# Kernel tuning notes

Hardware: AMD Instinct MI355X
Metric: run time of the kernel (lower is better)

Reference implementation:

```python
import jax, jax.numpy as jnp
import numpy as np

DIM = 1024
HEADS = 16
WIN = 16
N = WIN * WIN + 1  # 257, CLS + patches
NUM_REL = (2 * WIN - 1) * (2 * WIN - 1) + 3  # 964
B = 64


def _build_rel_pos_index(w):
    coords = np.stack(np.meshgrid(np.arange(w), np.arange(w), indexing='ij'))  # [2,w,w]
    cf = coords.reshape(2, -1)  # [2, w*w]
    rel = cf[:, :, None] - cf[:, None, :]  # [2, ww, ww]
    rel = rel.transpose(1, 2, 0).astype(np.int64)
    rel[..., 0] += w - 1
    rel[..., 1] += w - 1
    rel[..., 0] *= 2 * w - 1
    nrd = (2 * w - 1) * (2 * w - 1) + 3
    idx = np.zeros((w * w + 1, w * w + 1), dtype=np.int32)
    idx[1:, 1:] = rel.sum(-1)
    idx[0, :] = nrd - 3
    idx[:, 0] = nrd - 2
    idx[0, 0] = nrd - 1
    return idx


def setup_inputs() -> dict:
    key = jax.random.key(0)
    ks = jax.random.split(key, 4)
    x = jax.random.normal(ks[0], (B, N, DIM), dtype=jnp.float32)
    qkv_w = jax.random.normal(ks[1], (3 * DIM, DIM), dtype=jnp.float32) * 0.02
    q_bias = jnp.zeros((DIM,), dtype=jnp.float32)
    v_bias = jnp.zeros((DIM,), dtype=jnp.float32)
    rel_pos_table = jax.random.normal(ks[2], (NUM_REL, HEADS), dtype=jnp.float32) * 0.02
    proj_w = jax.random.normal(ks[3], (DIM, DIM), dtype=jnp.float32) * 0.02
    proj_b = jnp.zeros((DIM,), dtype=jnp.float32)
    rel_pos_index = jnp.asarray(_build_rel_pos_index(WIN))
    attn_mask = jnp.ones((B, N), dtype=jnp.bool_)
    return {"x": x, "qkv_w": qkv_w, "q_bias": q_bias, "v_bias": v_bias,
            "rel_pos_table": rel_pos_table, "proj_w": proj_w, "proj_b": proj_b,
            "rel_pos_index": rel_pos_index, "attn_mask": attn_mask}


def reference(x, qkv_w, q_bias, v_bias, rel_pos_table, proj_w, proj_b, rel_pos_index, attn_mask):
    b, n, c = x.shape
    head_dim = c // HEADS
    scale = head_dim ** -0.5
    # qkv with q_bias / zero k bias / v_bias
    qkv_bias = jnp.concatenate([q_bias, jnp.zeros_like(v_bias), v_bias])
    qkv = x @ qkv_w.T + qkv_bias  # [B,N,3C]
    qkv = qkv.reshape(b, n, 3, HEADS, head_dim).transpose(2, 0, 3, 1, 4)  # [3,B,H,N,d]
    q, k, v = qkv[0], qkv[1], qkv[2]
    # fp32 upcast for scores (qk_float=True)
    attn = jnp.einsum('bhqd,bhkd->bhqk', (q * scale).astype(jnp.float32), k.astype(jnp.float32))
    # gathered relative position bias: table[idx] -> [N,N,H] -> [H,N,N]
    rel_bias = rel_pos_table[rel_pos_index].transpose(2, 0, 1)  # [H,N,N]
    attn = attn + rel_bias[None].astype(attn.dtype)
    attn = jnp.where(attn_mask[:, None, None, :], attn, -jnp.inf)
    attn = jax.nn.softmax(attn, axis=-1).astype(x.dtype)
    out = jnp.einsum('bhqk,bhkd->bhqd', attn, v)  # [B,H,N,d]
    out = out.transpose(0, 2, 1, 3).reshape(b, n, -1)  # [B,N,C]
    return out @ proj_w.T + proj_b
```

## Files before the change

kernel.cpp:

```cpp
#include <hip/hip_runtime.h>


typedef __attribute__((ext_vector_type(8))) short bf16x8;
typedef __attribute__((ext_vector_type(4))) float f32x4;

#define MFMA16(A, B, C) __builtin_amdgcn_mfma_f32_16x16x32_bf16((A), (B), (C), 0, 0, 0)

#define MV   16448
#define KDIM 1024
#define SEQ  257
#define SEQP 272
#define VCOLS 320

__device__ __forceinline__ void gll16(void* lds, const void* g) {
    __builtin_amdgcn_global_load_lds(
        (const __attribute__((address_space(1))) void*)g,
        (__attribute__((address_space(3))) void*)lds,
        16, 0, 0);
}

__device__ __forceinline__ unsigned short f2bf(float f) {
    union { float f; unsigned int u; } x;
    x.f = f;
    unsigned int r = x.u + 0x7FFFu + ((x.u >> 16) & 1u);
    return (unsigned short)(r >> 16);
}

__global__ __launch_bounds__(256) void prep_k(
    const float* __restrict__ x, const float* __restrict__ wq, const float* __restrict__ wp,
    const float* __restrict__ table, const int* __restrict__ rpi,
    unsigned short* __restrict__ xb, unsigned short* __restrict__ wqb,
    unsigned short* __restrict__ wpb, float* __restrict__ biasb)
{
    const int XT = MV * KDIM / 4;
    const int QT = 3072 * KDIM / 4;
    const int PT = KDIM * KDIM / 4;
    const int total = XT + QT + PT;
    for (int i = blockIdx.x * blockDim.x + threadIdx.x; i < total; i += gridDim.x * blockDim.x) {
        const float4* s; unsigned short* d; int g;
        if (i < XT)            { s = (const float4*)x;  d = xb;  g = i; }
        else if (i < XT + QT)  { s = (const float4*)wq; d = wqb; g = i - XT; }
        else                   { s = (const float4*)wp; d = wpb; g = i - XT - QT; }
        float4 v = s[g];
        ushort4 u;
        u.x = f2bf(v.x); u.y = f2bf(v.y); u.z = f2bf(v.z); u.w = f2bf(v.w);
        *(ushort4*)(d + (size_t)g * 4) = u;
    }
    const int btotal = 16 * SEQP * SEQP;
    for (int i = blockIdx.x * blockDim.x + threadIdx.x; i < btotal; i += gridDim.x * blockDim.x) {
        int h = i / (SEQP * SEQP);
        int rem = i - h * (SEQP * SEQP);
        int q = rem / SEQP;
        int k = rem - q * SEQP;
        float v = 0.f;
        if (q < SEQ && k < SEQ) v = table[rpi[q * SEQ + k] * 16 + h];
        biasb[i] = v;
    }
}

template <int EPI>
__global__ __launch_bounds__(256) void gemm_bt(
    const unsigned short* __restrict__ A,
    const unsigned short* __restrict__ W,
    const float* __restrict__ f0,
    const float* __restrict__ f1,
    unsigned short* __restrict__ o0,
    unsigned short* __restrict__ o1,
    unsigned short* __restrict__ o2,
    float* __restrict__ fout)
{
    __shared__ __attribute__((aligned(16))) unsigned short As[128 * 64];
    __shared__ __attribute__((aligned(16))) unsigned short Bs[128 * 64];
    const int tid = threadIdx.x;
    const int lane = tid & 63;
    const int wid = tid >> 6;
    const int wr = wid >> 1, wc = wid & 1;
    const int m0 = blockIdx.y * 128;
    const int n0 = blockIdx.x * 128;

    const int swzel = (((lane & 7) ^ ((lane >> 3) & 7)) << 3);
    const size_t arow = (size_t)(m0 + wid * 32 + (lane >> 3)) * KDIM + swzel;
    const size_t wrow = (size_t)(n0 + wid * 32 + (lane >> 3)) * KDIM + swzel;

    f32x4 acc[4][4];
#pragma unroll
    for (int i = 0; i < 4; ++i)
#pragma unroll
        for (int j = 0; j < 4; ++j) acc[i][j] = 0.f;

    for (int kt = 0; kt < KDIM / 64; ++kt) {
        __syncthreads();
        const int kofs = kt * 64;
#pragma unroll
        for (int it = 0; it < 4; ++it) {
            gll16((char*)As + wid * 4096 + it * 1024, A + arow + (size_t)it * 8 * KDIM + kofs);
            gll16((char*)Bs + wid * 4096 + it * 1024, W + wrow + (size_t)it * 8 * KDIM + kofs);
        }
        asm volatile("s_waitcnt vmcnt(0)" ::: "memory");
        __syncthreads();
#pragma unroll
        for (int kk = 0; kk < 2; ++kk) {
            const int cbs = (kk * 64 + ((lane >> 4) << 4)) ^ ((lane & 7) << 4);
            bf16x8 av[4], bv[4];
#pragma unroll
            for (int mi = 0; mi < 4; ++mi) {
                const int R = wr * 64 + mi * 16 + (lane & 15);
                av[mi] = *(const bf16x8*)((const char*)As + R * 128 + cbs);
            }
#pragma unroll
            for (int ni = 0; ni < 4; ++ni) {
                const int R = wc * 64 + ni * 16 + (lane & 15);
                bv[ni] = *(const bf16x8*)((const char*)Bs + R * 128 + cbs);
            }
#pragma unroll
            for (int mi = 0; mi < 4; ++mi)
#pragma unroll
                for (int ni = 0; ni < 4; ++ni)
                    acc[mi][ni] = MFMA16(av[mi], bv[ni], acc[mi][ni]);
        }
    }

    if (EPI == 0) {
        const int which = n0 >> 10;
#pragma unroll
        for (int mi = 0; mi < 4; ++mi) {
#pragma unroll
            for (int j = 0; j < 4; ++j) {
                const int m = m0 + wr * 64 + mi * 16 + ((lane >> 4) << 2) + j;
                if (m >= MV) continue;
                const int b = m / SEQ;
                const int s = m - b * SEQ;
#pragma unroll
                for (int ni = 0; ni < 4; ++ni) {
                    const int n = n0 + wc * 64 + ni * 16 + (lane & 15);
                    const int hd = n & 1023;
                    const int h = hd >> 6, d = hd & 63;
                    const int bh = b * 16 + h;
                    const float v = acc[mi][ni][j];
                    if (which == 0)
                        o0[((size_t)bh * SEQP + s) * 64 + d] = f2bf((v + f0[hd]) * 0.125f);
                    else if (which == 1)
                        o1[((size_t)bh * SEQP + s) * 64 + d] = f2bf(v);
                    else
                        o2[((size_t)bh * 64 + d) * VCOLS + s] = f2bf(v + f1[hd]);
                }
            }
        }
    } else {
#pragma unroll
        for (int ni = 0; ni < 4; ++ni) {
            const int n = n0 + wc * 64 + ni * 16 + (lane & 15);
            const float pb = f0[n];
#pragma unroll
            for (int mi = 0; mi < 4; ++mi) {
#pragma unroll
                for (int j = 0; j < 4; ++j) {
                    const int m = m0 + wr * 64 + mi * 16 + ((lane >> 4) << 2) + j;
                    if (m < MV) fout[(size_t)m * KDIM + n] = acc[mi][ni][j] + pb;
                }
            }
        }
    }
}

__global__ __launch_bounds__(256) void attn_k(
    const unsigned short* __restrict__ qb, const unsigned short* __restrict__ kb,
    const unsigned short* __restrict__ vtb, const float* __restrict__ biasb,
    unsigned short* __restrict__ ao)
{
    __shared__ __attribute__((aligned(16))) unsigned short Ks[SEQP * 64];
    __shared__ __attribute__((aligned(16))) unsigned short Vs[64 * VCOLS];
    __shared__ __attribute__((aligned(16))) unsigned short Ps[4][640];

    const int bh = blockIdx.x;
    const int b = bh >> 4, h = bh & 15;
    const int tid = threadIdx.x;
    const int lane = tid & 63;
    const int wid = tid >> 6;

    {
        const unsigned short* kbase = kb + (size_t)bh * (SEQP * 64);
        const int swzel = (((lane & 7) ^ ((lane >> 3) & 7)) << 3);
        for (int c = wid; c < 34; c += 4)
            gll16((char*)Ks + c * 1024, kbase + (c * 8 + (lane >> 3)) * 64 + swzel);
        const char* vbase = (const char*)(vtb + (size_t)bh * (64 * VCOLS));
        for (int c = wid; c < 40; c += 4) {
            const int o = c * 1024 + lane * 16;
            const int r = o / 640;
            const int cbv = o - r * 640;
            const int csrc = cbv ^ ((r & 7) << 4);
            gll16((char*)Vs + c * 1024, vbase + r * 640 + csrc);
        }
    }
    asm volatile("s_waitcnt vmcnt(0)" ::: "memory");
    __syncthreads();

    const unsigned short* qbase = qb + (size_t)bh * (SEQP * 64);
    const float* bbase = biasb + (size_t)h * (SEQP * SEQP);

#pragma unroll 1
    for (int qt = wid; qt < 17; qt += 4) {
        const int qr0 = qt * 16;
        const bf16x8 aq0 = *(const bf16x8*)(qbase + (qr0 + (lane & 15)) * 64 + ((lane >> 4) << 3));
        const bf16x8 aq1 = *(const bf16x8*)(qbase + (qr0 + (lane & 15)) * 64 + 32 + ((lane >> 4) << 3));

        f32x4 s[17];
        const int cb0 = (((lane >> 4) << 4)) ^ ((lane & 7) << 4);
        const int cb1 = (64 + ((lane >> 4) << 4)) ^ ((lane & 7) << 4);
#pragma unroll
        for (int nt = 0; nt < 17; ++nt) {
            const int Rb = (nt * 16 + (lane & 15)) * 128;
            const bf16x8 bk0 = *(const bf16x8*)((const char*)Ks + Rb + cb0);
            const bf16x8 bk1 = *(const bf16x8*)((const char*)Ks + Rb + cb1);
            f32x4 z = 0.f;
            z = MFMA16(aq0, bk0, z);
            s[nt] = MFMA16(aq1, bk1, z);
        }

        float mx[4] = {-1e30f, -1e30f, -1e30f, -1e30f};
#pragma unroll
        for (int nt = 0; nt < 17; ++nt) {
            const int kcol = nt * 16 + (lane & 15);
            const bool ok = (nt < 16) || ((lane & 15) == 0);
#pragma unroll
            for (int j = 0; j < 4; ++j) {
                const int qr = qr0 + ((lane >> 4) << 2) + j;
                const float t = ok ? (s[nt][j] + bbase[qr * SEQP + kcol]) : -1e30f;
                s[nt][j] = t;
                mx[j] = fmaxf(mx[j], t);
            }
        }
#pragma unroll
        for (int j = 0; j < 4; ++j) {
            mx[j] = fmaxf(mx[j], __shfl_xor(mx[j], 1));
            mx[j] = fmaxf(mx[j], __shfl_xor(mx[j], 2));
            mx[j] = fmaxf(mx[j], __shfl_xor(mx[j], 4));
            mx[j] = fmaxf(mx[j], __shfl_xor(mx[j], 8));
        }
        float sm[4] = {0.f, 0.f, 0.f, 0.f};
#pragma unroll
        for (int nt = 0; nt < 17; ++nt)
#pragma unroll
            for (int j = 0; j < 4; ++j) {
                const float p = __expf(s[nt][j] - mx[j]);
                s[nt][j] = p;
                sm[j] += p;
            }
#pragma unroll
        for (int j = 0; j < 4; ++j) {
            sm[j] += __shfl_xor(sm[j], 1);
            sm[j] += __shfl_xor(sm[j], 2);
            sm[j] += __shfl_xor(sm[j], 4);
            sm[j] += __shfl_xor(sm[j], 8);
        }

        f32x4 o[4];
#pragma unroll
        for (int dt = 0; dt < 4; ++dt) o[dt] = 0.f;
        unsigned short* myP = &Ps[wid][0];
#pragma unroll
        for (int c = 0; c < 9; ++c) {
#pragma unroll
            for (int j = 0; j < 4; ++j) {
                const int row = ((lane >> 4) << 2) + j;
                myP[row * 40 + (lane & 15)] = f2bf(s[2 * c][j]);
                unsigned short hv = 0;
                if (c < 8) hv = f2bf(s[2 * c + 1][j]);
                myP[row * 40 + 16 + (lane & 15)] = hv;
            }
            asm volatile("s_waitcnt lgkmcnt(0)" ::: "memory");
            __builtin_amdgcn_sched_barrier(0);
            const bf16x8 pa = *(const bf16x8*)(myP + (lane & 15) * 40 + ((lane >> 4) << 3));
#pragma unroll
            for (int dt = 0; dt < 4; ++dt) {
                const int R = dt * 16 + (lane & 15);
                const int cbv = (c * 64 + ((lane >> 4) << 4)) ^ ((lane & 7) << 4);
                const bf16x8 bv = *(const bf16x8*)((const char*)Vs + R * 640 + cbv);
                o[dt] = MFMA16(pa, bv, o[dt]);
            }
        }

#pragma unroll
        for (int j = 0; j < 4; ++j) {
            const int qr = qr0 + ((lane >> 4) << 2) + j;
            if (qr < SEQ) {
                const float inv = 1.0f / sm[j];
                const size_t rowoff = ((size_t)(b * SEQ + qr)) * KDIM + h * 64;
#pragma unroll
                for (int dt = 0; dt < 4; ++dt)
                    ao[rowoff + dt * 16 + (lane & 15)] = f2bf(o[dt][j] * inv);
            }
        }
    }
}

extern "C" void kernel_launch(void* const* d_in, const int* in_sizes, int n_in,
                              void* d_out, int out_size, void* d_ws, size_t ws_size,
                              hipStream_t stream) {
    const float* x       = (const float*)d_in[0];
    const float* qkv_w   = (const float*)d_in[1];
    const float* q_bias  = (const float*)d_in[2];
    const float* v_bias  = (const float*)d_in[3];
    const float* table   = (const float*)d_in[4];
    const float* proj_w  = (const float*)d_in[5];
    const float* proj_b  = (const float*)d_in[6];
    const int*   rpi     = (const int*)d_in[7];
    float* out = (float*)d_out;

    char* w = (char*)d_ws;
    unsigned short* xb  = (unsigned short*)(w);
    unsigned short* wqb = (unsigned short*)(w + 33816576);
    unsigned short* wpb = (unsigned short*)(w + 40108032);
    float*          bb  = (float*)(w + 42205184);
    unsigned short* qbf = (unsigned short*)(w + 46940160);
    unsigned short* kbf = (unsigned short*)(w + 82591744);
    unsigned short* vtb = (unsigned short*)(w + 118243328);

    prep_k<<<2048, 256, 0, stream>>>(x, qkv_w, proj_w, table, rpi, xb, wqb, wpb, bb);
    gemm_bt<0><<<dim3(3072 / 128, 16512 / 128), 256, 0, stream>>>(
        xb, wqb, q_bias, v_bias, qbf, kbf, vtb, nullptr);
    attn_k<<<1024, 256, 0, stream>>>(qbf, kbf, vtb, bb, xb);
    gemm_bt<1><<<dim3(KDIM / 128, 16512 / 128), 256, 0, stream>>>(
        xb, wpb, proj_b, nullptr, nullptr, nullptr, nullptr, out);
}
```

Before: 322.7 us.

## Triple-buffer GEMM K-tiles with async global-to-LDS prefetch two stages ahead

The bf16 GEMM main loop moves from one 64-wide K tile per iteration, loaded synchronously behind two barriers, to 32-wide K tiles in a three-slot LDS ring. Loads are issued two tiles ahead and waited on with a partial vmcnt, so each iteration has one barrier. The LDS swizzle is reworked for the 64-byte row stride. The aim is to hide global load latency behind MFMA work, at the cost of more LDS per block (48 KB) and possibly lower occupancy.

```diff
diff --git a/kernel.cpp b/kernel.cpp
--- a/kernel.cpp
+++ b/kernel.cpp
@@ -69,8 +69,9 @@
     unsigned short* __restrict__ o2,
     float* __restrict__ fout)
 {
-    __shared__ __attribute__((aligned(16))) unsigned short As[128 * 64];
-    __shared__ __attribute__((aligned(16))) unsigned short Bs[128 * 64];
+    __shared__ __attribute__((aligned(16))) unsigned short smem_s[24576];
+    char* smem = (char*)smem_s;
+
     const int tid = threadIdx.x;
     const int lane = tid & 63;
     const int wid = tid >> 6;
@@ -78,9 +79,44 @@
     const int m0 = blockIdx.y * 128;
     const int n0 = blockIdx.x * 128;
 
-    const int swzel = (((lane & 7) ^ ((lane >> 3) & 7)) << 3);
-    const size_t arow = (size_t)(m0 + wid * 32 + (lane >> 3)) * KDIM + swzel;
-    const size_t wrow = (size_t)(n0 + wid * 32 + (lane >> 3)) * KDIM + swzel;
+    const int r4 = lane >> 2;
+    const int csw = ((lane & 3) ^ ((r4 >> 1) & 3)) << 3;
+    const size_t aS0 = (size_t)(m0 + (wid * 2 + 0) * 16 + r4) * KDIM + csw;
+    const size_t aS1 = (size_t)(m0 + (wid * 2 + 1) * 16 + r4) * KDIM + csw;
+    const size_t bS0 = (size_t)(n0 + (wid * 2 + 0) * 16 + r4) * KDIM + csw;
+    const size_t bS1 = (size_t)(n0 + (wid * 2 + 1) * 16 + r4) * KDIM + csw;
+
+    const int cbs = (((lane >> 4) ^ ((lane >> 1) & 3)) & 3) << 4;
+
+#define STAGE(P, KT) do { \
+    const size_t kofs_ = (size_t)(KT) * 32; \
+    gll16(smem + (P) * 16384 + (wid * 2 + 0) * 1024, A + aS0 + kofs_); \
+    gll16(smem + (P) * 16384 + (wid * 2 + 1) * 1024, A + aS1 + kofs_); \
+    gll16(smem + (P) * 16384 + 8192 + (wid * 2 + 0) * 1024, W + bS0 + kofs_); \
+    gll16(smem + (P) * 16384 + 8192 + (wid * 2 + 1) * 1024, W + bS1 + kofs_); \
+} while (0)
+
+#define COMPUTE(P) do { \
+    bf16x8 av[4], bv[4]; \
+    _Pragma("unroll") for (int mi = 0; mi < 4; ++mi) { \
+        const int R = wr * 64 + mi * 16 + (lane & 15); \
+        av[mi] = *(const bf16x8*)(smem + (P) * 16384 + R * 64 + cbs); } \
+    _Pragma("unroll") for (int ni = 0; ni < 4; ++ni) { \
+        const int R = wc * 64 + ni * 16 + (lane & 15); \
+        bv[ni] = *(const bf16x8*)(smem + (P) * 16384 + 8192 + R * 64 + cbs); } \
+    _Pragma("unroll") for (int mi = 0; mi < 4; ++mi) \
+        _Pragma("unroll") for (int ni = 0; ni < 4; ++ni) \
+            acc[mi][ni] = MFMA16(av[mi], bv[ni], acc[mi][ni]); \
+} while (0)
+
+#define ITER(P, PS, T, DOSTAGE, WAITN) do { \
+    asm volatile("s_waitcnt vmcnt(" #WAITN ")" ::: "memory"); \
+    asm volatile("" ::: "memory"); \
+    __builtin_amdgcn_s_barrier(); \
+    asm volatile("" ::: "memory"); \
+    if (DOSTAGE) STAGE(PS, (T) + 2); \
+    COMPUTE(P); \
+} while (0)
 
     f32x4 acc[4][4];
 #pragma unroll
@@ -88,37 +124,21 @@
 #pragma unroll
         for (int j = 0; j < 4; ++j) acc[i][j] = 0.f;
 
-    for (int kt = 0; kt < KDIM / 64; ++kt) {
-        __syncthreads();
-        const int kofs = kt * 64;
-#pragma unroll
-        for (int it = 0; it < 4; ++it) {
-            gll16((char*)As + wid * 4096 + it * 1024, A + arow + (size_t)it * 8 * KDIM + kofs);
-            gll16((char*)Bs + wid * 4096 + it * 1024, W + wrow + (size_t)it * 8 * KDIM + kofs);
-        }
-        asm volatile("s_waitcnt vmcnt(0)" ::: "memory");
-        __syncthreads();
-#pragma unroll
-        for (int kk = 0; kk < 2; ++kk) {
-            const int cbs = (kk * 64 + ((lane >> 4) << 4)) ^ ((lane & 7) << 4);
-            bf16x8 av[4], bv[4];
-#pragma unroll
-            for (int mi = 0; mi < 4; ++mi) {
-                const int R = wr * 64 + mi * 16 + (lane & 15);
-                av[mi] = *(const bf16x8*)((const char*)As + R * 128 + cbs);
-            }
-#pragma unroll
-            for (int ni = 0; ni < 4; ++ni) {
-                const int R = wc * 64 + ni * 16 + (lane & 15);
-                bv[ni] = *(const bf16x8*)((const char*)Bs + R * 128 + cbs);
-            }
-#pragma unroll
-            for (int mi = 0; mi < 4; ++mi)
-#pragma unroll
-                for (int ni = 0; ni < 4; ++ni)
-                    acc[mi][ni] = MFMA16(av[mi], bv[ni], acc[mi][ni]);
-        }
-    }
+    STAGE(0, 0);
+    STAGE(1, 1);
+
+#pragma unroll 1
+    for (int tb = 0; tb < 30; tb += 3) {
+        ITER(0, 2, tb + 0, true, 4);
+        ITER(1, 0, tb + 1, true, 4);
+        ITER(2, 1, tb + 2, true, 4);
+    }
+    ITER(0, 0, 30, false, 4);
+    ITER(1, 0, 31, false, 0);
+
+#undef ITER
+#undef COMPUTE
+#undef STAGE
 
     if (EPI == 0) {
         const int which = n0 >> 10;
@@ -317,9 +337,9 @@
     unsigned short* vtb = (unsigned short*)(w + 118243328);
 
     prep_k<<<2048, 256, 0, stream>>>(x, qkv_w, proj_w, table, rpi, xb, wqb, wpb, bb);
-    gemm_bt<0><<<dim3(3072 / 128, 16512 / 128), 256, 0, stream>>>(
+    gemm_bt<0><<<dim3(24, 129), 256, 0, stream>>>(
         xb, wqb, q_bias, v_bias, qbf, kbf, vtb, nullptr);
     attn_k<<<1024, 256, 0, stream>>>(qbf, kbf, vtb, bb, xb);
-    gemm_bt<1><<<dim3(KDIM / 128, 16512 / 128), 256, 0, stream>>>(
+    gemm_bt<1><<<dim3(8, 129), 256, 0, stream>>>(
         xb, wpb, proj_b, nullptr, nullptr, nullptr, nullptr, out);
 }
```

Result: slower. 349.1 us (+8.2%).
